# Kernel optimization log

Hardware: AMD Instinct MI355X
Metric: run time of the kernel (lower is better)

## Reference

```python
import jax, jax.numpy as jnp
import numpy as np

B, S, H, NH = 2, 1024, 1024, 16
HD = H // NH          # 64
SP = 0.05             # synaptic_plasticity
EPS = 1e-5            # torch LayerNorm default eps


def setup_inputs() -> dict:
    key = jax.random.key(0)
    ks = jax.random.split(key, 18)
    def lin(k, fin, fout):
        # torch Linear default init ~ U(-1/sqrt(fin), 1/sqrt(fin)); stored as [in, out]
        bound = 1.0 / np.sqrt(fin)
        return jax.random.uniform(k, (fin, fout), jnp.float32, -bound, bound)
    return {
        "query": jax.random.normal(ks[0], (B, S, H), jnp.float32),
        "key_t": jax.random.normal(ks[1], (B, S, H), jnp.float32),
        "value": jax.random.normal(ks[2], (B, S, H), jnp.float32),
        "Wq": lin(ks[3], H, H), "bq": jnp.zeros((H,), jnp.float32),
        "Wk": lin(ks[4], H, H), "bk": jnp.zeros((H,), jnp.float32),
        "Wv": lin(ks[5], H, H), "bv": jnp.zeros((H,), jnp.float32),
        # msb_weights init = ones*0.5 (+ tiny noise so grads are non-degenerate)
        "msb": 0.5 * jnp.ones((NH, HD, HD), jnp.float32)
               + 0.01 * jax.random.normal(ks[6], (NH, HD, HD), jnp.float32),
        "Ws1": lin(ks[7], H, H // 2), "bs1": jnp.zeros((H // 2,), jnp.float32),
        "Ws2": lin(ks[8], H // 2, H), "bs2": jnp.zeros((H,), jnp.float32),
        "Wo": lin(ks[9], H, H), "bo": jnp.zeros((H,), jnp.float32),
        "ln_g": jnp.ones((H,), jnp.float32),
        "ln_b": jnp.zeros((H,), jnp.float32),
    }


def reference(query, key_t, value, Wq, bq, Wk, bk, Wv, bv, msb,
              Ws1, bs1, Ws2, bs2, Wo, bo, ln_g, ln_b):
    b, s, h = query.shape
    # projections -> [b, nh, s, hd]
    Q = (query @ Wq + bq).reshape(b, s, NH, HD).transpose(0, 2, 1, 3)
    K = (key_t @ Wk + bk).reshape(b, s, NH, HD).transpose(0, 2, 1, 3)
    V = (value @ Wv + bv).reshape(b, s, NH, HD).transpose(0, 2, 1, 3)

    scores = jnp.einsum('bhqd,bhkd->bhqk', Q, K) / np.float32(np.sqrt(HD))

    # MSB sigmoid gate: per-head scalar = mean over (head_dim, head_dim)
    msb_h = msb.mean(axis=(1, 2))                              # [NH]
    enh = jax.nn.sigmoid(scores * msb_h[None, :, None, None])  # [b,nh,s,s]
    scores = scores * (1.0 + enh * SP)

    # input-specificity: MLP(mean over seq of query) -> sigmoid -> mean -> scalar per batch
    spec_in = query.mean(axis=1)                               # [b, h]
    h1 = jax.nn.relu(spec_in @ Ws1 + bs1)
    spec = jax.nn.sigmoid(h1 @ Ws2 + bs2).mean(axis=-1)        # [b]
    scores = scores * spec[:, None, None, None]

    w = jax.nn.softmax(scores, axis=-1)                        # dropout p=0 (eval)
    ctx = jnp.einsum('bhqk,bhkd->bhqd', w, V)
    ctx = ctx.transpose(0, 2, 1, 3).reshape(b, s, h)

    out = ctx @ Wo + bo + query                                # residual
    mu = out.mean(axis=-1, keepdims=True)
    var = out.var(axis=-1, keepdims=True)
    return (out - mu) / jnp.sqrt(var + EPS) * ln_g + ln_b
```

## Files before the change

### kernel.cpp

```cpp
#include <hip/hip_runtime.h>
#include <math.h>

#define BB   2
#define SS   1024
#define HH   1024
#define NHH  16
#define SPc  0.05f
#define EPSc 1e-5f

typedef unsigned short u16;
typedef unsigned int   u32;
using bf16x8 = __attribute__((ext_vector_type(8))) __bf16;
using f32x4  = __attribute__((ext_vector_type(4))) float;

__device__ __forceinline__ u16 f2bf(float f) {
    u32 u = __builtin_bit_cast(u32, f);
    u32 r = u + 0x7fffu + ((u >> 16) & 1u);
    return (u16)(r >> 16);
}

__device__ __forceinline__ void async16(void* lds, const void* g) {
    __builtin_amdgcn_global_load_lds((const __attribute__((address_space(1))) u32*)g,
                                     (__attribute__((address_space(3))) u32*)lds,
                                     16, 0, 0);
}

__device__ __forceinline__ bf16x8 ldb8(const u16* p) {
    return *(const bf16x8*)(const void*)p;
}

__global__ __launch_bounds__(256) void prep_kernel(
    const float* __restrict__ query, const float* __restrict__ key_t,
    const float* __restrict__ value,
    u16* __restrict__ Aq, u16* __restrict__ Ak, u16* __restrict__ Av,
    const float* __restrict__ W0, const float* __restrict__ W1,
    const float* __restrict__ W2, const float* __restrict__ W3,
    u16* __restrict__ T0, u16* __restrict__ T1,
    u16* __restrict__ T2, u16* __restrict__ T3,
    const float* __restrict__ msb, float* __restrict__ msbh,
    float* __restrict__ spp) {
    const int t = threadIdx.x;
    const int d = blockIdx.x;

    if (d < 6144) {
        const int which = d >> 11;
        const int bx    = d & 2047;
        const float* s; u16* dst;
        if (which == 0)      { s = query; dst = Aq; }
        else if (which == 1) { s = key_t; dst = Ak; }
        else                 { s = value; dst = Av; }
        const size_t i = ((size_t)bx * 256 + t) * 4;
        const float4 v = *(const float4*)(s + i);
        ushort4 o;
        o.x = f2bf(v.x); o.y = f2bf(v.y); o.z = f2bf(v.z); o.w = f2bf(v.w);
        *(ushort4*)(dst + i) = o;
        return;
    }
    if (d < 7168) {
        const int e  = d - 6144;
        const int wz = e >> 8;
        const int k0 = ((e >> 4) & 15) << 6;
        const int n0 = (e & 15) << 6;
        const float* W; u16* T;
        if (wz == 0)      { W = W0; T = T0; }
        else if (wz == 1) { W = W1; T = T1; }
        else if (wz == 2) { W = W2; T = T2; }
        else              { W = W3; T = T3; }
        __shared__ u16 tile[64][72];
        #pragma unroll
        for (int i = 0; i < 4; ++i) {
            const int chunk = i * 256 + t;
            const int r  = chunk >> 4;
            const int c4 = (chunk & 15) << 2;
            const float4 v = *(const float4*)(W + (size_t)(k0 + r) * 1024 + n0 + c4);
            tile[c4 + 0][r] = f2bf(v.x);
            tile[c4 + 1][r] = f2bf(v.y);
            tile[c4 + 2][r] = f2bf(v.z);
            tile[c4 + 3][r] = f2bf(v.w);
        }
        __syncthreads();
        #pragma unroll
        for (int i = 0; i < 4; ++i) {
            const int chunk = i * 256 + t;
            const int rn = chunk >> 4;
            const int ck = (chunk & 15) << 2;
            ushort4 o;
            o.x = tile[rn][ck + 0];
            o.y = tile[rn][ck + 1];
            o.z = tile[rn][ck + 2];
            o.w = tile[rn][ck + 3];
            *(ushort4*)(T + (size_t)(n0 + rn) * 1024 + k0 + ck) = o;
        }
        return;
    }
    if (d < 7184) {
        const int h = d - 7168;
        const float* p = msb + (size_t)h * 4096;
        float s = 0.f;
        for (int i = t; i < 4096; i += 256) s += p[i];
        __shared__ float red[256];
        red[t] = s;
        __syncthreads();
        for (int off = 128; off > 0; off >>= 1) {
            if (t < off) red[t] += red[t + off];
            __syncthreads();
        }
        if (t == 0) msbh[h] = red[0] * (1.f / 4096.f);
        return;
    }
    {
        const int e = d - 7184;
        const int x = e & 3;
        const int b = (e >> 2) & 1;
        const int z = e >> 3;
        const int h = x * 256 + t;
        const float* p = query + ((size_t)b * SS + (size_t)z * 128) * HH + h;
        float s = 0.f;
        for (int i = 0; i < 128; ++i) s += p[(size_t)i * HH];
        spp[((size_t)z * BB + b) * HH + h] = s;
    }
}

__global__ __launch_bounds__(256) void mlp2_part_kernel(
    const float* __restrict__ mp1, const float* __restrict__ bs1,
    const float* __restrict__ Ws2, float* __restrict__ mp2) {
    const int t   = threadIdx.x;
    const int oc  = blockIdx.x;
    const int kc2 = blockIdx.y;
    const int b   = blockIdx.z;
    __shared__ float x[128];
    if (t < 128) {
        const int j = kc2 * 128 + t;
        float a = bs1[j];
        #pragma unroll
        for (int kc = 0; kc < 8; ++kc) a += mp1[((size_t)kc * BB + b) * 512 + j];
        x[t] = fmaxf(a, 0.f);
    }
    __syncthreads();
    const int o = oc * 256 + t;
    float acc = 0.f;
    #pragma unroll 4
    for (int k2 = 0; k2 < 128; ++k2)
        acc += x[k2] * Ws2[(size_t)(kc2 * 128 + k2) * 1024 + o];
    mp2[((size_t)kc2 * BB + b) * 1024 + o] = acc;
}

template<int BM, int BN>
__device__ __forceinline__ void gemm_core(const u16* __restrict__ A,
                                          const u16* __restrict__ Bt,
                                          const float* __restrict__ bias,
                                          void* __restrict__ Cout, int mode,
                                          int m0, int n0) {
    constexpr int FI = BM / 32;
    constexpr int FJ = BN / 32;
    __shared__ u16 sA[2][BM * 32];
    __shared__ u16 sB[2][BN * 32];
    const int t  = threadIdx.x;
    const int l  = t & 63;
    const int wv = t >> 6;
    const int wm = wv >> 1, wn = wv & 1;
    const int wbase = t & ~63;
    const int ql = l & 15;
    const int g_ = l >> 4;

    f32x4 acc[FI][FJ];
    #pragma unroll
    for (int i = 0; i < FI; ++i)
        #pragma unroll
        for (int j = 0; j < FJ; ++j) acc[i][j] = (f32x4){0.f, 0.f, 0.f, 0.f};

    auto stage = [&](int buf, int k0) {
        #pragma unroll
        for (int ii = 0; ii < BM / 64; ++ii) {
            const int chunk = ii * 256 + t;
            const int r  = chunk >> 2, c = chunk & 3;
            const int cs = (c ^ ((r >> 1) & 3)) << 3;
            async16(&sA[buf][(ii * 256 + wbase) << 3],
                    A + (size_t)(m0 + r) * 1024 + k0 + cs);
        }
        #pragma unroll
        for (int ii = 0; ii < BN / 64; ++ii) {
            const int chunk = ii * 256 + t;
            const int r  = chunk >> 2, c = chunk & 3;
            const int cs = (c ^ ((r >> 1) & 3)) << 3;
            async16(&sB[buf][(ii * 256 + wbase) << 3],
                    Bt + (size_t)(n0 + r) * 1024 + k0 + cs);
        }
    };

    stage(0, 0);
    for (int kk = 0; kk < 32; ++kk) {
        const int cur = kk & 1;
        __syncthreads();
        if (kk < 31) stage(cur ^ 1, (kk + 1) << 5);
        const u16* bufA = sA[cur];
        const u16* bufB = sB[cur];
        bf16x8 af[FI], bg[FJ];
        #pragma unroll
        for (int i = 0; i < FI; ++i) {
            const int ra = wm * (BM / 2) + i * 16 + ql;
            af[i] = ldb8(bufA + ra * 32 + (((g_ ^ ((ra >> 1) & 3))) << 3));
        }
        #pragma unroll
        for (int j = 0; j < FJ; ++j) {
            const int rb = wn * (BN / 2) + j * 16 + ql;
            bg[j] = ldb8(bufB + rb * 32 + (((g_ ^ ((rb >> 1) & 3))) << 3));
        }
        __builtin_amdgcn_s_setprio(1);
        #pragma unroll
        for (int i = 0; i < FI; ++i)
            #pragma unroll
            for (int j = 0; j < FJ; ++j)
                acc[i][j] = __builtin_amdgcn_mfma_f32_16x16x32_bf16(af[i], bg[j], acc[i][j], 0, 0, 0);
        __builtin_amdgcn_s_setprio(0);
    }

    const int coll = ql;
    const int rowg = g_ << 2;
    #pragma unroll
    for (int j = 0; j < FJ; ++j) {
        const int n = n0 + wn * (BN / 2) + j * 16 + coll;
        const float bs = bias[n];
        #pragma unroll
        for (int i = 0; i < FI; ++i) {
            const int mb = m0 + wm * (BM / 2) + i * 16 + rowg;
            if (mode == 0) {
                float* C = (float*)Cout;
                #pragma unroll
                for (int rr = 0; rr < 4; ++rr)
                    C[(size_t)(mb + rr) * 1024 + n] = acc[i][j][rr] + bs;
            } else if (mode == 1) {
                u16* C = (u16*)Cout;
                #pragma unroll
                for (int rr = 0; rr < 4; ++rr)
                    C[(size_t)(mb + rr) * 1024 + n] = f2bf(acc[i][j][rr] + bs);
            } else {
                u16* C = (u16*)Cout;
                const int bI = mb >> 10;
                const int s  = mb & 1023;
                ushort4 o;
                o.x = f2bf(acc[i][j][0] + bs);
                o.y = f2bf(acc[i][j][1] + bs);
                o.z = f2bf(acc[i][j][2] + bs);
                o.w = f2bf(acc[i][j][3] + bs);
                *(ushort4*)(C + ((size_t)(bI * NHH + (n >> 6)) * 64 + (n & 63)) * 1024 + s) = o;
            }
        }
    }
}

__global__ __launch_bounds__(256, 3) void gemm_qkv_kernel(
    const u16* __restrict__ Aq, const u16* __restrict__ Ak, const u16* __restrict__ Av,
    const u16* __restrict__ WtQ, const u16* __restrict__ WtK, const u16* __restrict__ WtV,
    const float* __restrict__ bq, const float* __restrict__ bk, const float* __restrict__ bv,
    u16* __restrict__ Qbf, u16* __restrict__ Kbf, u16* __restrict__ Vt,
    const float* __restrict__ spp, const float* __restrict__ Ws1,
    float* __restrict__ mp1) {
    const int d = (int)blockIdx.x;
    if (d >= 768) {
        const int e  = d - 768;
        const int jc = e & 1;
        const int kc = (e >> 1) & 7;
        const int b  = e >> 4;
        const int t  = threadIdx.x;
        __shared__ float x[128];
        if (t < 128) {
            const int k = kc * 128 + t;
            float s = 0.f;
            #pragma unroll
            for (int z = 0; z < 8; ++z) s += spp[((size_t)z * BB + b) * HH + k];
            x[t] = s * (1.f / (float)SS);
        }
        __syncthreads();
        const int j = jc * 256 + t;
        float acc = 0.f;
        #pragma unroll 4
        for (int k2 = 0; k2 < 128; ++k2)
            acc += x[k2] * Ws1[(size_t)(kc * 128 + k2) * 512 + j];
        mp1[((size_t)kc * BB + b) * 512 + j] = acc;
        return;
    }
    const int g = (d & 7) * 96 + (d >> 3);
    const int n0 = (g & 7) << 7;
    const int m0 = ((g >> 3) & 31) << 6;
    const int zz = g >> 8;
    if (zz == 0)      gemm_core<64, 128>(Aq, WtQ, bq, Qbf, 1, m0, n0);
    else if (zz == 1) gemm_core<64, 128>(Ak, WtK, bk, Kbf, 1, m0, n0);
    else              gemm_core<64, 128>(Av, WtV, bv, Vt, 2, m0, n0);
}

__global__ __launch_bounds__(256, 3) void gemm_o_kernel(
    const u16* __restrict__ A, const u16* __restrict__ Bt,
    const float* __restrict__ bias, float* __restrict__ C) {
    const int d = (int)blockIdx.x + ((int)blockIdx.y << 4);
    const int g = (d & 7) * 64 + (d >> 3);
    const int n0 = (g & 15) << 6;
    const int m0 = (g >> 4) << 6;
    gemm_core<64, 64>(A, Bt, bias, C, 0, m0, n0);
}

__global__ __launch_bounds__(256, 2) void attn_mfma_kernel(
    const u16* __restrict__ Qbf, const u16* __restrict__ Kbf,
    const u16* __restrict__ Vt, const float* __restrict__ msbh,
    const float* __restrict__ mp2, const float* __restrict__ bs2,
    u16* __restrict__ ctx) {
    __shared__ u16 sK[2][4096];
    __shared__ u16 sV[2][4096];
    __shared__ float sred[256];

    const int t  = threadIdx.x;
    const int l  = t & 63;
    const int wv = t >> 6;
    const int wbase = t & ~63;
    const int qt = blockIdx.x, h = blockIdx.y, b = blockIdx.z;
    const int ql = l & 15;
    const int g_ = l >> 4;

    const u16* Kg = Kbf + (size_t)b * SS * HH + h * 64;
    const u16* Vg = Vt + (size_t)(b * NHH + h) * 64 * SS;

    const u16* qrow = Qbf + ((size_t)(b * SS + qt * 64 + wv * 16 + ql)) * HH + h * 64;
    const bf16x8 qf0 = ldb8(qrow + (g_ << 3));
    const bf16x8 qf1 = ldb8(qrow + ((4 + g_) << 3));

    int koff[2], vof[2], lof[2];
    #pragma unroll
    for (int ii = 0; ii < 2; ++ii) {
        const int chunk = ii * 256 + t;
        const int r = chunk >> 3, c = chunk & 7;
        const int rp = (r & 3) | (((r >> 2) & 3) << 3) | (((r >> 4) & 1) << 2) | (r & 32);
        const int cs = (c ^ (r & 7)) << 3;
        koff[ii] = rp * 1024 + cs;
        vof[ii]  = r * 1024 + cs;
        lof[ii]  = (ii * 256 + wbase) << 3;
    }

#define KVSTAGE(buf, kt)                                                        \
    {                                                                           \
        _Pragma("unroll")                                                       \
        for (int ii = 0; ii < 2; ++ii) {                                        \
            async16(sK[buf] + lof[ii], Kg + ((size_t)(kt) << 16) + koff[ii]);   \
            async16(sV[buf] + lof[ii], Vg + ((kt) << 6) + vof[ii]);             \
        }                                                                       \
    }

    KVSTAGE(0, 0)

    {
        float ssum = 0.f;
        #pragma unroll
        for (int i = 0; i < 4; ++i) {
            const int o = i * 256 + t;
            float a = bs2[o];
            #pragma unroll
            for (int kc = 0; kc < 4; ++kc) a += mp2[((size_t)kc * BB + b) * 1024 + o];
            ssum += 1.f / (1.f + __expf(-a));
        }
        sred[t] = ssum;
        __syncthreads();
        for (int off = 128; off > 0; off >>= 1) {
            if (t < off) sred[t] += sred[t + off];
            __syncthreads();
        }
    }
    const float sp = sred[0] * (1.f / 1024.f);

    const float mh = msbh[h] * 0.125f;
    const float c2 = 0.125f * sp;
    const float c3 = 0.125f * sp * SPc;
    const float Ac = c2 + 0.5f * c3;
    const float Bc = 0.25f * c3 * mh;
    const float Dc = c3 * mh * mh * mh * (1.f / 48.f);

    f32x4 oacc[4];
    #pragma unroll
    for (int dt = 0; dt < 4; ++dt) oacc[dt] = (f32x4){0.f, 0.f, 0.f, 0.f};
    float lsum = 0.f;

    for (int kt = 0; kt < 16; ++kt) {
        const int cur = kt & 1;
        __syncthreads();
        if (kt < 15) KVSTAGE(cur ^ 1, kt + 1)

        const u16* bufK = sK[cur];
        const u16* bufV = sV[cur];

        f32x4 sc[4];
        __builtin_amdgcn_s_setprio(1);
        #pragma unroll
        for (int f = 0; f < 4; ++f) {
            const int r = (f << 4) + ql;
            bf16x8 kfa = ldb8(bufK + r * 64 + ((g_ ^ (r & 7)) << 3));
            bf16x8 kfb = ldb8(bufK + r * 64 + (((4 + g_) ^ (r & 7)) << 3));
            f32x4 z = (f32x4){0.f, 0.f, 0.f, 0.f};
            z = __builtin_amdgcn_mfma_f32_16x16x32_bf16(kfa, qf0, z, 0, 0, 0);
            z = __builtin_amdgcn_mfma_f32_16x16x32_bf16(kfb, qf1, z, 0, 0, 0);
            sc[f] = z;
        }
        __builtin_amdgcn_s_setprio(0);

        bf16x8 pf0, pf1;
        #pragma unroll
        for (int f = 0; f < 4; ++f) {
            #pragma unroll
            for (int rr = 0; rr < 4; ++rr) {
                const float raw = sc[f][rr];
                const float r2 = raw * raw;
                const float tt = fmaf(-Dc, r2, Bc);
                const float v  = fmaf(tt, r2, Ac * raw);
                const float p  = __expf(v);
                lsum += p;
                const __bf16 pbv = (__bf16)p;
                if (f == 0)      pf0[rr] = pbv;
                else if (f == 1) pf0[4 + rr] = pbv;
                else if (f == 2) pf1[rr] = pbv;
                else             pf1[4 + rr] = pbv;
            }
        }

        __builtin_amdgcn_s_setprio(1);
        #pragma unroll
        for (int dt = 0; dt < 4; ++dt) {
            const int r = (dt << 4) + ql;
            bf16x8 vf0 = ldb8(bufV + r * 64 + ((g_ ^ (r & 7)) << 3));
            bf16x8 vf1 = ldb8(bufV + r * 64 + (((4 + g_) ^ (r & 7)) << 3));
            oacc[dt] = __builtin_amdgcn_mfma_f32_16x16x32_bf16(pf0, vf0, oacc[dt], 0, 0, 0);
            oacc[dt] = __builtin_amdgcn_mfma_f32_16x16x32_bf16(pf1, vf1, oacc[dt], 0, 0, 0);
        }
        __builtin_amdgcn_s_setprio(0);
    }
#undef KVSTAGE

    lsum += __shfl_xor(lsum, 16);
    lsum += __shfl_xor(lsum, 32);

    float linv[4];
    #pragma unroll
    for (int rr = 0; rr < 4; ++rr) linv[rr] = 1.f / __shfl(lsum, (g_ << 2) + rr);

    #pragma unroll
    for (int rr = 0; rr < 4; ++rr) {
        const int q = qt * 64 + wv * 16 + (g_ << 2) + rr;
        u16* crow = ctx + ((size_t)(b * SS + q)) * HH + h * 64;
        #pragma unroll
        for (int dt = 0; dt < 4; ++dt)
            crow[dt * 16 + ql] = f2bf(oacc[dt][rr] * linv[rr]);
    }
}

__global__ __launch_bounds__(256) void ln_kernel(
    const float* __restrict__ X, const float* __restrict__ qin,
    const float* __restrict__ g, const float* __restrict__ be, float* __restrict__ out) {
    const int row = blockIdx.x;
    const int t   = threadIdx.x;
    const int d4  = t << 2;
    const float4 x4 = *(const float4*)(X + (size_t)row * HH + d4);
    const float4 q4 = *(const float4*)(qin + (size_t)row * HH + d4);
    float4 v;
    v.x = x4.x + q4.x;
    v.y = x4.y + q4.y;
    v.z = x4.z + q4.z;
    v.w = x4.w + q4.w;
    float s  = v.x + v.y + v.z + v.w;
    float sq = v.x * v.x + v.y * v.y + v.z * v.z + v.w * v.w;
    for (int off = 1; off < 64; off <<= 1) {
        s  += __shfl_xor(s, off);
        sq += __shfl_xor(sq, off);
    }
    __shared__ float rs[4], rq[4];
    const int w = t >> 6;
    if ((t & 63) == 0) { rs[w] = s; rq[w] = sq; }
    __syncthreads();
    s  = rs[0] + rs[1] + rs[2] + rs[3];
    sq = rq[0] + rq[1] + rq[2] + rq[3];
    const float mu   = s * (1.f / (float)HH);
    const float var  = sq * (1.f / (float)HH) - mu * mu;
    const float rstd = rsqrtf(var + EPSc);
    const float4 g4 = *(const float4*)(g + d4);
    const float4 b4 = *(const float4*)(be + d4);
    float4 o;
    o.x = (v.x - mu) * rstd * g4.x + b4.x;
    o.y = (v.y - mu) * rstd * g4.y + b4.y;
    o.z = (v.z - mu) * rstd * g4.z + b4.z;
    o.w = (v.w - mu) * rstd * g4.w + b4.w;
    *(float4*)(out + (size_t)row * HH + d4) = o;
}

extern "C" void kernel_launch(void* const* d_in, const int* in_sizes, int n_in,
                              void* d_out, int out_size, void* d_ws, size_t ws_size,
                              hipStream_t stream) {
    (void)in_sizes; (void)n_in; (void)out_size; (void)ws_size;
    const float* query = (const float*)d_in[0];
    const float* key_t = (const float*)d_in[1];
    const float* value = (const float*)d_in[2];
    const float* Wq  = (const float*)d_in[3];
    const float* bq  = (const float*)d_in[4];
    const float* Wk  = (const float*)d_in[5];
    const float* bk  = (const float*)d_in[6];
    const float* Wv  = (const float*)d_in[7];
    const float* bv  = (const float*)d_in[8];
    const float* msb = (const float*)d_in[9];
    const float* Ws1 = (const float*)d_in[10];
    const float* bs1 = (const float*)d_in[11];
    const float* Ws2 = (const float*)d_in[12];
    const float* bs2 = (const float*)d_in[13];
    const float* Wo  = (const float*)d_in[14];
    const float* bo  = (const float*)d_in[15];
    const float* lng = (const float*)d_in[16];
    const float* lnb = (const float*)d_in[17];
    float* out = (float*)d_out;

    char* p = (char*)d_ws;
    u16* Aq    = (u16*)p;
    u16* Ak    = Aq + 2097152;
    u16* Av    = Ak + 2097152;
    u16* WtQ   = Av + 2097152;
    u16* WtK   = WtQ + 1048576;
    u16* WtV   = WtK + 1048576;
    u16* WtO   = WtV + 1048576;
    u16* Qbf   = WtO + 1048576;
    u16* Kbf   = Qbf + 2097152;
    u16* Vt    = Kbf + 2097152;
    u16* ctxbf = Vt + 2097152;
    float* Obuf = (float*)Aq;
    float* spp   = (float*)(p + 36 * 1024 * 1024);
    float* mp1   = spp + 16384;
    float* mp2   = mp1 + 8192;
    float* msbh  = mp2 + 8192;

    prep_kernel<<<dim3(7248), 256, 0, stream>>>(
        query, key_t, value, Aq, Ak, Av,
        Wq, Wk, Wv, Wo, WtQ, WtK, WtV, WtO, msb, msbh, spp);

    gemm_qkv_kernel<<<dim3(800), 256, 0, stream>>>(
        Aq, Ak, Av, WtQ, WtK, WtV, bq, bk, bv, Qbf, Kbf, Vt, spp, Ws1, mp1);

    mlp2_part_kernel<<<dim3(4, 4, BB), 256, 0, stream>>>(mp1, bs1, Ws2, mp2);

    attn_mfma_kernel<<<dim3(16, NHH, BB), 256, 0, stream>>>(
        Qbf, Kbf, Vt, msbh, mp2, bs2, ctxbf);

    gemm_o_kernel<<<dim3(16, 32), 256, 0, stream>>>(ctxbf, WtO, bo, Obuf);

    ln_kernel<<<dim3(BB * SS), 256, 0, stream>>>(Obuf, query, lng, lnb, out);
}
```

Baseline: 95.21 us.

## Double GEMM K-step to 64 and replace block reduction with wave shuffles

The shared GEMM core now stages 64-wide K slices instead of 32, using an 8-way XOR swizzle. This halves the number of K iterations and barriers, and each iteration issues two MFMAs per fragment pair. In the attention kernel, every wave now computes the specificity scalar redundantly with a 64-lane shuffle reduction. That replaces the LDS tree reduction and its eight __syncthreads. The cost is double the GEMM LDS footprint, which may reduce occupancy, and 4x redundant global reads of mp2 per block.

```diff
diff --git a/kernel.cpp b/kernel.cpp
--- a/kernel.cpp
+++ b/kernel.cpp
@@ -153,8 +153,8 @@
                                           int m0, int n0) {
     constexpr int FI = BM / 32;
     constexpr int FJ = BN / 32;
-    __shared__ u16 sA[2][BM * 32];
-    __shared__ u16 sB[2][BN * 32];
+    __shared__ u16 sA[2][BM * 64];
+    __shared__ u16 sB[2][BN * 64];
     const int t  = threadIdx.x;
     const int l  = t & 63;
     const int wv = t >> 6;
@@ -171,47 +171,53 @@
 
     auto stage = [&](int buf, int k0) {
         #pragma unroll
-        for (int ii = 0; ii < BM / 64; ++ii) {
+        for (int ii = 0; ii < BM / 32; ++ii) {
             const int chunk = ii * 256 + t;
-            const int r  = chunk >> 2, c = chunk & 3;
-            const int cs = (c ^ ((r >> 1) & 3)) << 3;
+            const int r  = chunk >> 3, c = chunk & 7;
+            const int cs = (c ^ (r & 7)) << 3;
             async16(&sA[buf][(ii * 256 + wbase) << 3],
                     A + (size_t)(m0 + r) * 1024 + k0 + cs);
         }
         #pragma unroll
-        for (int ii = 0; ii < BN / 64; ++ii) {
+        for (int ii = 0; ii < BN / 32; ++ii) {
             const int chunk = ii * 256 + t;
-            const int r  = chunk >> 2, c = chunk & 3;
-            const int cs = (c ^ ((r >> 1) & 3)) << 3;
+            const int r  = chunk >> 3, c = chunk & 7;
+            const int cs = (c ^ (r & 7)) << 3;
             async16(&sB[buf][(ii * 256 + wbase) << 3],
                     Bt + (size_t)(n0 + r) * 1024 + k0 + cs);
         }
     };
 
     stage(0, 0);
-    for (int kk = 0; kk < 32; ++kk) {
+    for (int kk = 0; kk < 16; ++kk) {
         const int cur = kk & 1;
         __syncthreads();
-        if (kk < 31) stage(cur ^ 1, (kk + 1) << 5);
+        if (kk < 15) stage(cur ^ 1, (kk + 1) << 6);
         const u16* bufA = sA[cur];
         const u16* bufB = sB[cur];
-        bf16x8 af[FI], bg[FJ];
+        bf16x8 af[FI][2], bg[FJ][2];
         #pragma unroll
         for (int i = 0; i < FI; ++i) {
             const int ra = wm * (BM / 2) + i * 16 + ql;
-            af[i] = ldb8(bufA + ra * 32 + (((g_ ^ ((ra >> 1) & 3))) << 3));
+            const u16* base = bufA + ra * 64;
+            af[i][0] = ldb8(base + ((g_ ^ (ra & 7)) << 3));
+            af[i][1] = ldb8(base + (((4 + g_) ^ (ra & 7)) << 3));
         }
         #pragma unroll
         for (int j = 0; j < FJ; ++j) {
             const int rb = wn * (BN / 2) + j * 16 + ql;
-            bg[j] = ldb8(bufB + rb * 32 + (((g_ ^ ((rb >> 1) & 3))) << 3));
+            const u16* base = bufB + rb * 64;
+            bg[j][0] = ldb8(base + ((g_ ^ (rb & 7)) << 3));
+            bg[j][1] = ldb8(base + (((4 + g_) ^ (rb & 7)) << 3));
         }
         __builtin_amdgcn_s_setprio(1);
         #pragma unroll
         for (int i = 0; i < FI; ++i)
             #pragma unroll
-            for (int j = 0; j < FJ; ++j)
-                acc[i][j] = __builtin_amdgcn_mfma_f32_16x16x32_bf16(af[i], bg[j], acc[i][j], 0, 0, 0);
+            for (int j = 0; j < FJ; ++j) {
+                acc[i][j] = __builtin_amdgcn_mfma_f32_16x16x32_bf16(af[i][0], bg[j][0], acc[i][j], 0, 0, 0);
+                acc[i][j] = __builtin_amdgcn_mfma_f32_16x16x32_bf16(af[i][1], bg[j][1], acc[i][j], 0, 0, 0);
+            }
         __builtin_amdgcn_s_setprio(0);
     }
 
@@ -306,7 +312,6 @@
     u16* __restrict__ ctx) {
     __shared__ u16 sK[2][4096];
     __shared__ u16 sV[2][4096];
-    __shared__ float sred[256];
 
     const int t  = threadIdx.x;
     const int l  = t & 63;
@@ -346,24 +351,18 @@
 
     KVSTAGE(0, 0)
 
-    {
-        float ssum = 0.f;
-        #pragma unroll
-        for (int i = 0; i < 4; ++i) {
-            const int o = i * 256 + t;
-            float a = bs2[o];
-            #pragma unroll
-            for (int kc = 0; kc < 4; ++kc) a += mp2[((size_t)kc * BB + b) * 1024 + o];
-            ssum += 1.f / (1.f + __expf(-a));
-        }
-        sred[t] = ssum;
-        __syncthreads();
-        for (int off = 128; off > 0; off >>= 1) {
-            if (t < off) sred[t] += sred[t + off];
-            __syncthreads();
-        }
-    }
-    const float sp = sred[0] * (1.f / 1024.f);
+    float ssum = 0.f;
+    #pragma unroll
+    for (int j = 0; j < 16; ++j) {
+        const int o = (j << 6) + l;
+        float a = bs2[o];
+        #pragma unroll
+        for (int kc = 0; kc < 4; ++kc) a += mp2[((size_t)kc * BB + b) * 1024 + o];
+        ssum += 1.f / (1.f + __expf(-a));
+    }
+    #pragma unroll
+    for (int off = 1; off < 64; off <<= 1) ssum += __shfl_xor(ssum, off);
+    const float sp = ssum * (1.f / 1024.f);
 
     const float mh = msbh[h] * 0.125f;
     const float c2 = 0.125f * sp;
```

Result: slower. 97.15 us (+2.0%).

## Triple-buffer LDS stages with explicit vmcnt waits and warp-local spec reduction

Applied to the files above, without the earlier changes.

Moves the GEMM core and the attention kernel from double to triple LDS buffering. The next tile is issued before waiting, and an explicit s_waitcnt vmcnt leaves that tile's async loads in flight while the current one is consumed, so a single barrier per iteration replaces the earlier __syncthreads. The aim is to overlap global-to-LDS copies with MFMA work and drop one barrier per step. The attention kernel also computes the specificity scalar with a per-wave shuffle reduction, with every wave doing the full sum redundantly, instead of a shared-memory tree with many barriers. In exchange LDS use rises, which may lower occupancy, and correctness depends on the vmcnt counts matching the number of outstanding loads.

```diff
diff --git a/kernel.cpp b/kernel.cpp
--- a/kernel.cpp
+++ b/kernel.cpp
@@ -153,8 +153,9 @@
                                           int m0, int n0) {
     constexpr int FI = BM / 32;
     constexpr int FJ = BN / 32;
-    __shared__ u16 sA[2][BM * 32];
-    __shared__ u16 sB[2][BN * 32];
+    constexpr int NL = BM / 64 + BN / 64;
+    __shared__ u16 sA[3][BM * 32];
+    __shared__ u16 sB[3][BN * 32];
     const int t  = threadIdx.x;
     const int l  = t & 63;
     const int wv = t >> 6;
@@ -190,9 +191,14 @@
 
     stage(0, 0);
     for (int kk = 0; kk < 32; ++kk) {
-        const int cur = kk & 1;
-        __syncthreads();
-        if (kk < 31) stage(cur ^ 1, (kk + 1) << 5);
+        const int cur = kk % 3;
+        if (kk < 31) {
+            stage((kk + 1) % 3, (kk + 1) << 5);
+            asm volatile("s_waitcnt vmcnt(%0)" :: "i"(NL) : "memory");
+        } else {
+            asm volatile("s_waitcnt vmcnt(0)" ::: "memory");
+        }
+        __builtin_amdgcn_s_barrier();
         const u16* bufA = sA[cur];
         const u16* bufB = sB[cur];
         bf16x8 af[FI], bg[FJ];
@@ -304,9 +310,8 @@
     const u16* __restrict__ Vt, const float* __restrict__ msbh,
     const float* __restrict__ mp2, const float* __restrict__ bs2,
     u16* __restrict__ ctx) {
-    __shared__ u16 sK[2][4096];
-    __shared__ u16 sV[2][4096];
-    __shared__ float sred[256];
+    __shared__ u16 sK[3][4096];
+    __shared__ u16 sV[3][4096];
 
     const int t  = threadIdx.x;
     const int l  = t & 63;
@@ -346,24 +351,18 @@
 
     KVSTAGE(0, 0)
 
-    {
-        float ssum = 0.f;
-        #pragma unroll
-        for (int i = 0; i < 4; ++i) {
-            const int o = i * 256 + t;
-            float a = bs2[o];
-            #pragma unroll
-            for (int kc = 0; kc < 4; ++kc) a += mp2[((size_t)kc * BB + b) * 1024 + o];
-            ssum += 1.f / (1.f + __expf(-a));
-        }
-        sred[t] = ssum;
-        __syncthreads();
-        for (int off = 128; off > 0; off >>= 1) {
-            if (t < off) sred[t] += sred[t + off];
-            __syncthreads();
-        }
-    }
-    const float sp = sred[0] * (1.f / 1024.f);
+    float ssum = 0.f;
+    #pragma unroll
+    for (int j = 0; j < 16; ++j) {
+        const int o = (j << 6) + l;
+        float a = bs2[o];
+        #pragma unroll
+        for (int kc = 0; kc < 4; ++kc) a += mp2[((size_t)kc * BB + b) * 1024 + o];
+        ssum += 1.f / (1.f + __expf(-a));
+    }
+    #pragma unroll
+    for (int off = 1; off < 64; off <<= 1) ssum += __shfl_xor(ssum, off);
+    const float sp = ssum * (1.f / 1024.f);
 
     const float mh = msbh[h] * 0.125f;
     const float c2 = 0.125f * sp;
@@ -378,9 +377,14 @@
     float lsum = 0.f;
 
     for (int kt = 0; kt < 16; ++kt) {
-        const int cur = kt & 1;
-        __syncthreads();
-        if (kt < 15) KVSTAGE(cur ^ 1, kt + 1)
+        const int cur = kt % 3;
+        if (kt < 15) {
+            KVSTAGE((kt + 1) % 3, kt + 1)
+            asm volatile("s_waitcnt vmcnt(4)" ::: "memory");
+        } else {
+            asm volatile("s_waitcnt vmcnt(0)" ::: "memory");
+        }
+        __builtin_amdgcn_s_barrier();
 
         const u16* bufK = sK[cur];
         const u16* bufV = sV[cur];
```

Result: no change. 94.29 us (-1.0%).
